# Optimization experiments

Hardware: AMD Instinct MI355X
Metric: run time of the kernel (lower is better)

Reference implementation:

```python
import jax, jax.numpy as jnp
import numpy as np

N = 100_000      # num nodes
E = 1_600_000    # num edges
F_IN = 128       # input feature dim
H = 128          # hidden dim
C = 16           # num classes
R = 5            # num relations


def setup_inputs() -> dict:
    key = jax.random.key(0)
    ks = jax.random.split(key, 12)
    x = jax.random.normal(ks[0], (N, F_IN), jnp.float32)
    edge_index = jax.random.randint(ks[1], (2, E), 0, N, dtype=jnp.int64)
    edge_weight = jax.random.uniform(ks[2], (E,), jnp.float32)
    edge_type = jax.random.randint(ks[3], (E,), 0, R, dtype=jnp.int64)
    # RGCNConv params (no basis decomposition): per-relation weight, root, bias
    s1 = 1.0 / np.sqrt(F_IN).astype(np.float32)
    s2 = 1.0 / np.sqrt(H).astype(np.float32)
    W1 = jax.random.normal(ks[4], (R, F_IN, H), jnp.float32) * s1
    root1 = jax.random.normal(ks[5], (F_IN, H), jnp.float32) * s1
    b1 = jnp.zeros((H,), jnp.float32)
    W2 = jax.random.normal(ks[6], (R, H, C), jnp.float32) * s2
    root2 = jax.random.normal(ks[7], (H, C), jnp.float32) * s2
    b2 = jnp.zeros((C,), jnp.float32)
    return {"x": x, "edge_index": edge_index, "edge_weight": edge_weight,
            "edge_type": edge_type, "W1": W1, "root1": root1, "b1": b1,
            "W2": W2, "root2": root2, "b2": b2}


def _rgcn_conv(x, src, dst, ew, et, W, root, b):
    """WeightedRGCNConv: per-relation weighted mean aggregation + relation matmul.

    Equivalent to the torch loop over relations: mask edges of type r,
    propagate with aggr='mean' (PyG RGCNConv default) on messages
    edge_weight * x[src], then h_r @ W[r], summed over r; plus root & bias.
    Vectorized by scattering into (dst, relation) buckets.
    """
    n, r = x.shape[0], W.shape[0]
    m = x[src] * ew[:, None]                       # [E, d_in] messages
    seg = dst * r + et                             # bucket = (dst node, relation)
    sums = jax.ops.segment_sum(m, seg, num_segments=n * r).reshape(n, r, -1)
    cnt = jax.ops.segment_sum(jnp.ones_like(ew), seg, num_segments=n * r)
    cnt = cnt.reshape(n, r, 1)
    agg = sums / jnp.maximum(cnt, 1.0)             # mean; 0 for empty buckets
    out = jnp.einsum('nri,rio->no', agg, W)        # sum_r H_r @ W_r
    return out + x @ root + b


def reference(x, edge_index, edge_weight, edge_type, W1, root1, b1, W2, root2, b2):
    src, dst = edge_index[0], edge_index[1]
    h = _rgcn_conv(x, src, dst, edge_weight, edge_type, W1, root1, b1)
    h = jax.nn.relu(h)  # dropout is identity in eval mode
    out = _rgcn_conv(h, src, dst, edge_weight, edge_type, W2, root2, b2)
    return jax.nn.log_softmax(out, axis=1)
```

## Files before the change

### kernel.cpp

```cpp
#include <hip/hip_runtime.h>

#define N_NODES 100000
#define N_EDGES 1600000
#define N_REL   5
#define NCOARSE  391
#define CAP      8192

using bf16x8 = __attribute__((ext_vector_type(8))) short;
using f32x4  = __attribute__((ext_vector_type(4))) float;
using f32x2  = __attribute__((ext_vector_type(2))) float;

__device__ __forceinline__ unsigned short f2bf(float f) {
    unsigned int u = __float_as_uint(f);
    u += 0x7fffu + ((u >> 16) & 1u);
    return (unsigned short)(u >> 16);
}
__device__ __forceinline__ float bfu(unsigned short u) { return __uint_as_float((unsigned int)u << 16); }
__device__ __forceinline__ float bflo(unsigned int p) { return __uint_as_float(p << 16); }
__device__ __forceinline__ float bfhi(unsigned int p) { return __uint_as_float(p & 0xffff0000u); }

__global__ __launch_bounds__(1024) void partition_append(
    const int* __restrict__ src, const int* __restrict__ dstv,
    const float* __restrict__ ew, const int* __restrict__ et,
    int* __restrict__ ccur, int2* __restrict__ pe) {
    __shared__ int lh[512];
    __shared__ int lb[512];
    int tid = threadIdx.x;
    if (tid < 512) lh[tid] = 0;
    __syncthreads();
    int base = blockIdx.x * 4096;
    int key[4], rank[4], meta[4];
    float w[4];
    #pragma unroll
    for (int i = 0; i < 4; ++i) {
        int e = base + i * 1024 + tid;
        key[i] = -1;
        if (e < N_EDGES) {
            int d = dstv[e];
            key[i] = d >> 8;
            meta[i] = src[e] | (et[e] << 17) | ((d & 255) << 20);
            w[i] = ew[e];
            rank[i] = atomicAdd(&lh[key[i]], 1);
        }
    }
    __syncthreads();
    if (tid < 512) {
        int c = lh[tid];
        lb[tid] = (c && tid < NCOARSE) ? atomicAdd(&ccur[tid], c) : 0;
    }
    __syncthreads();
    #pragma unroll
    for (int i = 0; i < 4; ++i)
        if (key[i] >= 0) {
            int pos = lb[key[i]] + rank[i];
            if (pos < CAP)
                pe[((size_t)key[i] << 13) + pos] = make_int2(meta[i], __float_as_int(w[i]));
        }
}

__global__ __launch_bounds__(512) void cscan(const int* __restrict__ ccur,
                                             int* __restrict__ cstart) {
    __shared__ int lds[512];
    int tid = threadIdx.x;
    int v = (tid < NCOARSE) ? ccur[tid] : 0;
    lds[tid] = v;
    __syncthreads();
    for (int d = 1; d < 512; d <<= 1) {
        int t = (tid >= d) ? lds[tid - d] : 0;
        __syncthreads();
        lds[tid] += t;
        __syncthreads();
    }
    if (tid < NCOARSE) cstart[tid] = lds[tid] - v;
}

__global__ __launch_bounds__(1024) void bucket_sort(
    const int* __restrict__ ccnt, const int* __restrict__ cstart,
    const int2* __restrict__ pe, int2* __restrict__ edges,
    int* __restrict__ nbase, int2* __restrict__ nbp) {
    int cb = blockIdx.x;
    int node0 = cb << 8;
    if (node0 >= N_NODES) return;
    int nNodes = N_NODES - node0; if (nNodes > 256) nNodes = 256;
    int nf = nNodes * N_REL;
    __shared__ int hist[1280];
    __shared__ int cur[1280];
    __shared__ int wtot[16];
    __shared__ int woff[16];
    int tid = threadIdx.x;
    int wid = tid >> 6, lane = tid & 63;
    int cnt = ccnt[cb]; if (cnt > CAP) cnt = CAP;
    int gbase = cstart[cb];
    const int2* my = pe + ((size_t)cb << 13);

    for (int i = tid; i < nf; i += 1024) hist[i] = 0;
    __syncthreads();
    for (int i = tid; i < cnt; i += 1024) {
        int m = my[i].x;
        atomicAdd(&hist[((m >> 20) & 255) * N_REL + ((m >> 17) & 7)], 1);
    }
    __syncthreads();

    int t0 = tid * 2;
    int a0 = (t0 + 0 < nf) ? hist[t0 + 0] : 0;
    int a1 = (t0 + 1 < nf) ? hist[t0 + 1] : 0;
    int s = a0 + a1;
    int incl = s;
    #pragma unroll
    for (int d = 1; d < 64; d <<= 1) {
        int t = __shfl_up(incl, d);
        if (lane >= d) incl += t;
    }
    if (lane == 63) wtot[wid] = incl;
    __syncthreads();
    if (wid == 0 && lane < 16) {
        int v = wtot[lane];
        int inc2 = v;
        #pragma unroll
        for (int d = 1; d < 16; d <<= 1) {
            int t = __shfl_up(inc2, d);
            if (lane >= d) inc2 += t;
        }
        woff[lane] = inc2 - v;
    }
    __syncthreads();
    int excl = incl - s + woff[wid];
    if (t0 + 0 < nf) cur[t0 + 0] = excl;
    excl += a0;
    if (t0 + 1 < nf) cur[t0 + 1] = excl;
    __syncthreads();

    for (int i = tid; i < nNodes; i += 1024) {
        int b = i * N_REL;
        int c0 = cur[b];
        int deg = cur[b + 4] + hist[b + 4] - c0;
        nbase[node0 + i] = gbase + c0;
        nbp[node0 + i] = make_int2(0, deg);
    }
    __syncthreads();

    for (int i = tid; i < cnt; i += 1024) {
        int2 r = my[i];
        int fb = ((r.x >> 20) & 255) * N_REL + ((r.x >> 17) & 7);
        int pos = gbase + atomicAdd(&cur[fb], 1);
        float wf = __int_as_float(r.y) / (float)hist[fb];
        edges[pos] = make_int2(r.x & 0xFFFFF, __float_as_int(wf));
    }
}

__global__ void cvt_feat(const float* __restrict__ x, ushort* __restrict__ xh) {
    int i = blockIdx.x * blockDim.x + threadIdx.x;
    if (i >= (N_NODES * 128) / 4) return;
    float4 v = reinterpret_cast<const float4*>(x)[i];
    ushort4 o;
    o.x = f2bf(v.x); o.y = f2bf(v.y); o.z = f2bf(v.z); o.w = f2bf(v.w);
    reinterpret_cast<ushort4*>(xh)[i] = o;
}

__global__ void cvt_weights(const float* __restrict__ W1, const float* __restrict__ root1,
                            const float* __restrict__ W2, const float* __restrict__ root2,
                            ushort* __restrict__ Wt1b, ushort* __restrict__ Wt2s) {
    int i = blockIdx.x * blockDim.x + threadIdx.x;
    if (i < 768 * 128) {
        int o640 = i >> 7, k = i & 127;
        int seg = o640 >> 7, o = o640 & 127;
        float v;
        if (seg < 5) v = W1[((size_t)seg * 128 + k) * 128 + o];
        else         v = root1[k * 128 + o];
        int j = ((o & 7) << 4) | (o >> 3);
        Wt1b[((size_t)(seg * 128 + j)) * 128 + k] = f2bf(v);
    } else if (i < 768 * 128 + 96 * 128) {
        int ii = i - 768 * 128;
        int o = ii >> 7, k = ii & 127;
        float v = (o < 16) ? root2[k * 16 + o]
                           : W2[((size_t)((o >> 4) - 1) * 128 + k) * 16 + (o & 15)];
        Wt2s[ii] = f2bf(v);
    }
}

__global__ __launch_bounds__(256) void gemmZ(
    const ushort* __restrict__ xh, const ushort* __restrict__ Wt1b,
    unsigned char* __restrict__ Zq, ushort* __restrict__ Zroot) {
    __shared__ ushort As[64 * 128];
    __shared__ ushort Bs[128 * 128];
    const int tid = threadIdx.x, lane = tid & 63, wave = tid >> 6;
    const int m0 = blockIdx.x * 64;
    const int seg0 = blockIdx.y * 3;

    #pragma unroll
    for (int u = 0; u < 4; ++u) {
        int idx = tid + u * 256;
        int row = idx >> 4, slot = idx & 15;
        int gr = m0 + row; if (gr >= N_NODES) gr = N_NODES - 1;
        float4 v = *reinterpret_cast<const float4*>(xh + (size_t)gr * 128 + slot * 8);
        int byte = row * 256 + ((slot ^ (row & 15)) << 4);
        *reinterpret_cast<float4*>(reinterpret_cast<char*>(As) + byte) = v;
    }

    for (int si = 0; si < 3; ++si) {
        int seg = seg0 + si;
        #pragma unroll
        for (int u = 0; u < 8; ++u) {
            int idx = tid + u * 256;
            int row = idx >> 4, slot = idx & 15;
            float4 v = *reinterpret_cast<const float4*>(
                Wt1b + ((size_t)(seg * 128 + row)) * 128 + slot * 8);
            int byte = row * 256 + ((slot ^ (row & 15)) << 4);
            *reinterpret_cast<float4*>(reinterpret_cast<char*>(Bs) + byte) = v;
        }
        __syncthreads();

        f32x4 acc[8] = {};
        #pragma unroll
        for (int ks = 0; ks < 4; ++ks) {
            bf16x8 af, bfr[8];
            {
                int row = wave * 16 + (lane & 15);
                int slot = ks * 4 + (lane >> 4);
                int byte = row * 256 + ((slot ^ (row & 15)) << 4);
                af = *reinterpret_cast<const bf16x8*>(
                    reinterpret_cast<const char*>(As) + byte);
            }
            #pragma unroll
            for (int nn = 0; nn < 8; ++nn) {
                int row = nn * 16 + (lane & 15);
                int slot = ks * 4 + (lane >> 4);
                int byte = row * 256 + ((slot ^ (row & 15)) << 4);
                bfr[nn] = *reinterpret_cast<const bf16x8*>(
                    reinterpret_cast<const char*>(Bs) + byte);
            }
            #pragma unroll
            for (int nn = 0; nn < 8; ++nn)
                acc[nn] = __builtin_amdgcn_mfma_f32_16x16x32_bf16(
                    af, bfr[nn], acc[nn], 0, 0, 0);
        }

        int p = lane & 15;
        int rloc = m0 + wave * 16 + (lane >> 4) * 4;
        if (seg < 5) {
            #pragma unroll
            for (int q = 0; q < 4; ++q) {
                int row = rloc + q;
                if (row < N_NODES) {
                    int d0 = __builtin_amdgcn_cvt_pk_fp8_f32(acc[0][q], acc[1][q], 0, false);
                    d0 = __builtin_amdgcn_cvt_pk_fp8_f32(acc[2][q], acc[3][q], d0, true);
                    int d1 = __builtin_amdgcn_cvt_pk_fp8_f32(acc[4][q], acc[5][q], 0, false);
                    d1 = __builtin_amdgcn_cvt_pk_fp8_f32(acc[6][q], acc[7][q], d1, true);
                    *reinterpret_cast<int2*>(Zq + (size_t)row * 640 + seg * 128 + p * 8) =
                        make_int2(d0, d1);
                }
            }
        } else {
            #pragma unroll
            for (int q = 0; q < 4; ++q) {
                int row = rloc + q;
                if (row < N_NODES) {
                    uint4 v;
                    v.x = (unsigned)f2bf(acc[0][q]) | ((unsigned)f2bf(acc[1][q]) << 16);
                    v.y = (unsigned)f2bf(acc[2][q]) | ((unsigned)f2bf(acc[3][q]) << 16);
                    v.z = (unsigned)f2bf(acc[4][q]) | ((unsigned)f2bf(acc[5][q]) << 16);
                    v.w = (unsigned)f2bf(acc[6][q]) | ((unsigned)f2bf(acc[7][q]) << 16);
                    *reinterpret_cast<uint4*>(Zroot + (size_t)row * 128 + p * 8) = v;
                }
            }
        }
        __syncthreads();
    }
}

__global__ __launch_bounds__(256) void gather2(
    const ushort* __restrict__ Zq,
    const int2* __restrict__ edges,
    const int* __restrict__ nbase, const int2* __restrict__ nbp,
    const ushort* __restrict__ Zroot,
    const float* __restrict__ b1,
    ushort* __restrict__ h) {
    int n = __builtin_amdgcn_readfirstlane(blockIdx.x * 4 + (threadIdx.x >> 6));
    int lane = threadIdx.x & 63;
    int o0  = __builtin_amdgcn_readfirstlane(nbase[n]);
    int deg = __builtin_amdgcn_readfirstlane(nbp[n].y);
    f32x2 acc = {0.f, 0.f};

    if (deg <= 64) {
        int2 er = (lane < deg) ? edges[o0 + lane] : make_int2(0, 0);
        int deg8 = (deg + 7) & ~7;
        for (int j = 0; j < deg8; j += 8) {
            unsigned short q[8];
            float w[8];
            #pragma unroll
            for (int u = 0; u < 8; ++u) {
                int m = __builtin_amdgcn_readlane(er.x, j + u);
                int s5 = (m & 0x1FFFF) * 5 + ((m >> 17) & 7);
                q[u] = Zq[((size_t)s5 << 6) + lane];
            }
            #pragma unroll
            for (int u = 0; u < 8; ++u)
                w[u] = __uint_as_float(__builtin_amdgcn_readlane(er.y, j + u));
            #pragma unroll
            for (int u = 0; u < 8; ++u) {
                f32x2 f = __builtin_amdgcn_cvt_pk_f32_fp8((int)q[u], false);
                f32x2 ws = {w[u], w[u]};
                acc = __builtin_elementwise_fma(ws, f, acc);
            }
        }
    } else {
        for (int base = o0; base < o0 + deg; base += 64) {
            int rem = o0 + deg - base;
            int mcap = rem > 64 ? 64 : rem;
            int2 er = (lane < mcap) ? edges[base + lane] : make_int2(0, 0);
            int m8 = (mcap + 7) & ~7;
            for (int j = 0; j < m8; j += 8) {
                unsigned short q[8];
                float w[8];
                #pragma unroll
                for (int u = 0; u < 8; ++u) {
                    int m = __builtin_amdgcn_readlane(er.x, j + u);
                    int s5 = (m & 0x1FFFF) * 5 + ((m >> 17) & 7);
                    q[u] = Zq[((size_t)s5 << 6) + lane];
                }
                #pragma unroll
                for (int u = 0; u < 8; ++u)
                    w[u] = __uint_as_float(__builtin_amdgcn_readlane(er.y, j + u));
                #pragma unroll
                for (int u = 0; u < 8; ++u) {
                    f32x2 f = __builtin_amdgcn_cvt_pk_f32_fp8((int)q[u], false);
                    f32x2 ws = {w[u], w[u]};
                    acc = __builtin_elementwise_fma(ws, f, acc);
                }
            }
        }
    }

    unsigned int zr = reinterpret_cast<const unsigned int*>(Zroot)[(size_t)n * 64 + lane];
    float h0 = fmaxf(bflo(zr) + acc.x + b1[2 * lane], 0.f);
    float h1 = fmaxf(bfhi(zr) + acc.y + b1[2 * lane + 1], 0.f);
    reinterpret_cast<unsigned int*>(h)[(size_t)n * 64 + lane] =
        (unsigned int)f2bf(h0) | ((unsigned int)f2bf(h1) << 16);
}

__global__ __launch_bounds__(256) void gemmYh(
    const ushort* __restrict__ h, const ushort* __restrict__ Wt2,
    ushort* __restrict__ Yh) {
    __shared__ ushort As[128 * 128];
    __shared__ ushort Bs[96 * 128];
    const int tid = threadIdx.x, lane = tid & 63, wave = tid >> 6;
    const int m0 = blockIdx.x * 128;

    #pragma unroll
    for (int u = 0; u < 8; ++u) {
        int idx = tid + u * 256;
        int row = idx >> 4, slot = idx & 15;
        int gr = m0 + row; if (gr >= N_NODES) gr = N_NODES - 1;
        float4 v = *reinterpret_cast<const float4*>(h + (size_t)gr * 128 + slot * 8);
        int byte = row * 256 + ((slot ^ (row & 15)) << 4);
        *reinterpret_cast<float4*>(reinterpret_cast<char*>(As) + byte) = v;
    }
    #pragma unroll
    for (int u = 0; u < 6; ++u) {
        int idx = tid + u * 256;
        int row = idx >> 4, slot = idx & 15;
        float4 v = *reinterpret_cast<const float4*>(Wt2 + (size_t)row * 128 + slot * 8);
        int byte = row * 256 + ((slot ^ (row & 15)) << 4);
        *reinterpret_cast<float4*>(reinterpret_cast<char*>(Bs) + byte) = v;
    }
    __syncthreads();

    f32x4 acc2[2][6] = {};
    #pragma unroll
    for (int ks = 0; ks < 4; ++ks) {
        bf16x8 af[2], bfr[6];
        #pragma unroll
        for (int m = 0; m < 2; ++m) {
            int row = wave * 32 + m * 16 + (lane & 15);
            int slot = ks * 4 + (lane >> 4);
            int byte = row * 256 + ((slot ^ (row & 15)) << 4);
            af[m] = *reinterpret_cast<const bf16x8*>(
                reinterpret_cast<const char*>(As) + byte);
        }
        #pragma unroll
        for (int nn = 0; nn < 6; ++nn) {
            int row = nn * 16 + (lane & 15);
            int slot = ks * 4 + (lane >> 4);
            int byte = row * 256 + ((slot ^ (row & 15)) << 4);
            bfr[nn] = *reinterpret_cast<const bf16x8*>(
                reinterpret_cast<const char*>(Bs) + byte);
        }
        #pragma unroll
        for (int m = 0; m < 2; ++m)
            #pragma unroll
            for (int nn = 0; nn < 6; ++nn)
                acc2[m][nn] = __builtin_amdgcn_mfma_f32_16x16x32_bf16(
                    af[m], bfr[nn], acc2[m][nn], 0, 0, 0);
    }

    #pragma unroll
    for (int m = 0; m < 2; ++m) {
        int rloc = m0 + wave * 32 + m * 16 + (lane >> 4) * 4;
        #pragma unroll
        for (int nn = 0; nn < 6; ++nn) {
            int c = nn * 16 + (lane & 15);
            #pragma unroll
            for (int q = 0; q < 4; ++q) {
                int row = rloc + q;
                if (row < N_NODES) Yh[(size_t)row * 96 + c] = f2bf(acc2[m][nn][q]);
            }
        }
    }
}

__global__ __launch_bounds__(256) void agg2_softmax(
    const ushort* __restrict__ Yh, const int2* __restrict__ edges,
    const int* __restrict__ nbase, const int2* __restrict__ nbp,
    const float* __restrict__ b2, float* __restrict__ out) {
    int wave = threadIdx.x >> 6, lane = threadIdx.x & 63;
    int q = lane >> 4, c = lane & 15;
    int n = (blockIdx.x * 4 + wave) * 4 + q;
    int nn = (n < N_NODES) ? n : N_NODES - 1;
    int o0 = nbase[nn];
    int deg = nbp[nn].y;

    float val = bfu(Yh[(size_t)nn * 96 + c]) + b2[c];

    for (int b = 0; b < deg; b += 16) {
        int2 er = (b + c < deg) ? edges[o0 + b + c] : make_int2(0, 0);
        #pragma unroll
        for (int j = 0; j < 16; ++j) {
            int m = __shfl(er.x, q * 16 + j);
            float w = __uint_as_float(__shfl(er.y, q * 16 + j));
            int s = m & 0x1FFFF;
            int rel = (m >> 17) & 7;
            val = fmaf(w, bfu(Yh[(size_t)s * 96 + 16 + rel * 16 + c]), val);
        }
    }

    float mx = val;
    #pragma unroll
    for (int i = 1; i < 16; i <<= 1) mx = fmaxf(mx, __shfl_xor(mx, i));
    float ex = expf(val - mx);
    float ssum = ex;
    #pragma unroll
    for (int i = 1; i < 16; i <<= 1) ssum += __shfl_xor(ssum, i);
    float r = val - mx - logf(ssum);
    if (n < N_NODES) out[(size_t)n * 16 + c] = r;
}

extern "C" void kernel_launch(void* const* d_in, const int* in_sizes, int n_in,
                              void* d_out, int out_size, void* d_ws, size_t ws_size,
                              hipStream_t stream) {
    const float* x     = (const float*)d_in[0];
    const int*   ei    = (const int*)d_in[1];
    const int*   src   = ei;
    const int*   dst   = ei + N_EDGES;
    const float* ew    = (const float*)d_in[2];
    const int*   et    = (const int*)d_in[3];
    const float* W1    = (const float*)d_in[4];
    const float* root1 = (const float*)d_in[5];
    const float* b1    = (const float*)d_in[6];
    const float* W2    = (const float*)d_in[7];
    const float* root2 = (const float*)d_in[8];
    const float* b2    = (const float*)d_in[9];
    float* out = (float*)d_out;

    char* ws = (char*)d_ws;
    int*    ccur    = (int*)ws;
    int*    cstart  = (int*)(ws + 2048);
    int*    nbase   = (int*)(ws + 4096);
    int2*   nbp     = (int2*)(ws + 404096);
    int2*   edges   = (int2*)(ws + 1204096);
    ushort* xh      = (ushort*)(ws + 14004096);
    ushort* Wt1b    = (ushort*)(ws + 39604096);
    ushort* Wt2s    = (ushort*)(ws + 39800704);
    ushort* Zroot   = (ushort*)(ws + 39825280);
    ushort* h       = (ushort*)(ws + 65425280);
    unsigned char* Zq = (unsigned char*)(ws + 91025280);
    ushort* Yh      = (ushort*)(ws + 155025280);
    int2*   pe      = (int2*)(ws + 174225280);

    cvt_feat<<<((N_NODES * 128 / 4) + 255) / 256, 256, 0, stream>>>(x, xh);
    cvt_weights<<<((768 * 128 + 96 * 128) + 255) / 256, 256, 0, stream>>>(
        W1, root1, W2, root2, Wt1b, Wt2s);

    hipMemsetAsync(ccur, 0, 2048, stream);
    partition_append<<<(N_EDGES + 4095) / 4096, 1024, 0, stream>>>(src, dst, ew, et, ccur, pe);
    cscan<<<1, 512, 0, stream>>>(ccur, cstart);
    bucket_sort<<<NCOARSE, 1024, 0, stream>>>(ccur, cstart, pe, edges, nbase, nbp);

    gemmZ<<<dim3((N_NODES + 63) / 64, 2), 256, 0, stream>>>(xh, Wt1b, Zq, Zroot);

    gather2<<<N_NODES / 4, 256, 0, stream>>>(
        (const ushort*)Zq, edges, nbase, nbp, Zroot, b1, h);

    gemmYh<<<(N_NODES + 127) / 128, 256, 0, stream>>>(h, Wt2s, Yh);

    agg2_softmax<<<(N_NODES + 15) / 16, 256, 0, stream>>>(
        Yh, edges, nbase, nbp, b2, out);
}
```

Baseline: 181.9 us.

## Fuse layer-1 gather with layer-2 projection GEMM via shared-memory h tile

Merges the layer-1 gather kernel and the separate h·W2 GEMM into one kernel. Each 1024-thread block gathers 16 nodes, writes their bf16 hidden rows into a swizzled LDS tile, and six waves then run MFMA against W2 read straight from global memory to produce Yh. This removes the h round-trip through HBM and one launch. In exchange, blocks become much larger, ten of sixteen waves sit idle during the GEMM phase, and a block-wide barrier now ties the gather waves together.

After: 189.3 us. +4.1%, slower.

```diff
diff --git a/kernel.cpp b/kernel.cpp
--- a/kernel.cpp
+++ b/kernel.cpp
@@ -268,15 +268,17 @@
     }
 }
 
-__global__ __launch_bounds__(256) void gather2(
+__global__ __launch_bounds__(1024) void gather2Y(
     const ushort* __restrict__ Zq,
     const int2* __restrict__ edges,
     const int* __restrict__ nbase, const int2* __restrict__ nbp,
     const ushort* __restrict__ Zroot,
     const float* __restrict__ b1,
-    ushort* __restrict__ h) {
-    int n = __builtin_amdgcn_readfirstlane(blockIdx.x * 4 + (threadIdx.x >> 6));
-    int lane = threadIdx.x & 63;
+    const ushort* __restrict__ Wt2,
+    ushort* __restrict__ Yh) {
+    __shared__ ushort hs[16 * 128];
+    int wid = threadIdx.x >> 6, lane = threadIdx.x & 63;
+    int n = __builtin_amdgcn_readfirstlane(blockIdx.x * 16 + wid);
     int o0  = __builtin_amdgcn_readfirstlane(nbase[n]);
     int deg = __builtin_amdgcn_readfirstlane(nbp[n].y);
     f32x2 acc = {0.f, 0.f};
@@ -334,76 +336,39 @@
     unsigned int zr = reinterpret_cast<const unsigned int*>(Zroot)[(size_t)n * 64 + lane];
     float h0 = fmaxf(bflo(zr) + acc.x + b1[2 * lane], 0.f);
     float h1 = fmaxf(bfhi(zr) + acc.y + b1[2 * lane + 1], 0.f);
-    reinterpret_cast<unsigned int*>(h)[(size_t)n * 64 + lane] =
-        (unsigned int)f2bf(h0) | ((unsigned int)f2bf(h1) << 16);
-}
-
-__global__ __launch_bounds__(256) void gemmYh(
-    const ushort* __restrict__ h, const ushort* __restrict__ Wt2,
-    ushort* __restrict__ Yh) {
-    __shared__ ushort As[128 * 128];
-    __shared__ ushort Bs[96 * 128];
-    const int tid = threadIdx.x, lane = tid & 63, wave = tid >> 6;
-    const int m0 = blockIdx.x * 128;
-
-    #pragma unroll
-    for (int u = 0; u < 8; ++u) {
-        int idx = tid + u * 256;
-        int row = idx >> 4, slot = idx & 15;
-        int gr = m0 + row; if (gr >= N_NODES) gr = N_NODES - 1;
-        float4 v = *reinterpret_cast<const float4*>(h + (size_t)gr * 128 + slot * 8);
-        int byte = row * 256 + ((slot ^ (row & 15)) << 4);
-        *reinterpret_cast<float4*>(reinterpret_cast<char*>(As) + byte) = v;
-    }
-    #pragma unroll
-    for (int u = 0; u < 6; ++u) {
-        int idx = tid + u * 256;
-        int row = idx >> 4, slot = idx & 15;
-        float4 v = *reinterpret_cast<const float4*>(Wt2 + (size_t)row * 128 + slot * 8);
-        int byte = row * 256 + ((slot ^ (row & 15)) << 4);
-        *reinterpret_cast<float4*>(reinterpret_cast<char*>(Bs) + byte) = v;
-    }
-    __syncthreads();
-
-    f32x4 acc2[2][6] = {};
-    #pragma unroll
-    for (int ks = 0; ks < 4; ++ks) {
-        bf16x8 af[2], bfr[6];
-        #pragma unroll
-        for (int m = 0; m < 2; ++m) {
-            int row = wave * 32 + m * 16 + (lane & 15);
-            int slot = ks * 4 + (lane >> 4);
-            int byte = row * 256 + ((slot ^ (row & 15)) << 4);
-            af[m] = *reinterpret_cast<const bf16x8*>(
-                reinterpret_cast<const char*>(As) + byte);
-        }
-        #pragma unroll
-        for (int nn = 0; nn < 6; ++nn) {
-            int row = nn * 16 + (lane & 15);
-            int slot = ks * 4 + (lane >> 4);
-            int byte = row * 256 + ((slot ^ (row & 15)) << 4);
-            bfr[nn] = *reinterpret_cast<const bf16x8*>(
-                reinterpret_cast<const char*>(Bs) + byte);
-        }
-        #pragma unroll
-        for (int m = 0; m < 2; ++m)
-            #pragma unroll
-            for (int nn = 0; nn < 6; ++nn)
-                acc2[m][nn] = __builtin_amdgcn_mfma_f32_16x16x32_bf16(
-                    af[m], bfr[nn], acc2[m][nn], 0, 0, 0);
-    }
-
-    #pragma unroll
-    for (int m = 0; m < 2; ++m) {
-        int rloc = m0 + wave * 32 + m * 16 + (lane >> 4) * 4;
-        #pragma unroll
-        for (int nn = 0; nn < 6; ++nn) {
-            int c = nn * 16 + (lane & 15);
-            #pragma unroll
-            for (int q = 0; q < 4; ++q) {
-                int row = rloc + q;
-                if (row < N_NODES) Yh[(size_t)row * 96 + c] = f2bf(acc2[m][nn][q]);
-            }
+    unsigned int packed = (unsigned int)f2bf(h0) | ((unsigned int)f2bf(h1) << 16);
+    {
+        int s16 = lane >> 2;
+        int byte = wid * 256 + ((s16 ^ (wid & 15)) << 4) + ((lane * 4) & 15);
+        *reinterpret_cast<unsigned int*>(reinterpret_cast<char*>(hs) + byte) = packed;
+    }
+    __syncthreads();
+
+    if (wid < 6) {
+        f32x4 a2 = {};
+        #pragma unroll
+        for (int ks = 0; ks < 4; ++ks) {
+            bf16x8 af, bfr;
+            {
+                int row = lane & 15;
+                int slot = ks * 4 + (lane >> 4);
+                int byte = row * 256 + ((slot ^ (row & 15)) << 4);
+                af = *reinterpret_cast<const bf16x8*>(
+                    reinterpret_cast<const char*>(hs) + byte);
+            }
+            {
+                int brow = wid * 16 + (lane & 15);
+                bfr = *reinterpret_cast<const bf16x8*>(
+                    Wt2 + (size_t)brow * 128 + (ks * 4 + (lane >> 4)) * 8);
+            }
+            a2 = __builtin_amdgcn_mfma_f32_16x16x32_bf16(af, bfr, a2, 0, 0, 0);
+        }
+        int c = wid * 16 + (lane & 15);
+        #pragma unroll
+        for (int q = 0; q < 4; ++q) {
+            int row = (lane >> 4) * 4 + q;
+            int gn = blockIdx.x * 16 + row;
+            Yh[(size_t)gn * 96 + c] = f2bf(a2[q]);
         }
     }
 }
@@ -471,10 +436,9 @@
     ushort* Wt1b    = (ushort*)(ws + 39604096);
     ushort* Wt2s    = (ushort*)(ws + 39800704);
     ushort* Zroot   = (ushort*)(ws + 39825280);
-    ushort* h       = (ushort*)(ws + 65425280);
-    unsigned char* Zq = (unsigned char*)(ws + 91025280);
-    ushort* Yh      = (ushort*)(ws + 155025280);
-    int2*   pe      = (int2*)(ws + 174225280);
+    unsigned char* Zq = (unsigned char*)(ws + 65425280);
+    ushort* Yh      = (ushort*)(ws + 129425280);
+    int2*   pe      = (int2*)(ws + 148625280);
 
     cvt_feat<<<((N_NODES * 128 / 4) + 255) / 256, 256, 0, stream>>>(x, xh);
     cvt_weights<<<((768 * 128 + 96 * 128) + 255) / 256, 256, 0, stream>>>(
@@ -487,10 +451,8 @@
 
     gemmZ<<<dim3((N_NODES + 63) / 64, 2), 256, 0, stream>>>(xh, Wt1b, Zq, Zroot);
 
-    gather2<<<N_NODES / 4, 256, 0, stream>>>(
-        (const ushort*)Zq, edges, nbase, nbp, Zroot, b1, h);
-
-    gemmYh<<<(N_NODES + 127) / 128, 256, 0, stream>>>(h, Wt2s, Yh);
+    gather2Y<<<N_NODES / 16, 1024, 0, stream>>>(
+        (const ushort*)Zq, edges, nbase, nbp, Zroot, b1, Wt2s, Yh);
 
     agg2_softmax<<<(N_NODES + 15) / 16, 256, 0, stream>>>(
         Yh, edges, nbase, nbp, b2, out);
```
